# Performance work log

Measured on AMD Instinct MI355X. Metric: run time of the kernel, lower is better.

The kernel has to match this reference:

```python
import jax, jax.numpy as jnp
import numpy as np

H, W = 56, 56
N = H * W
C = 2
THETA_ALPHA = 160.0
THETA_BETA = 3.0
THETA_GAMMA = 3.0
NUM_ITERATIONS = 10


def setup_inputs() -> dict:
    key = jax.random.key(0)
    k1, k2, k3, k4 = jax.random.split(key, 4)
    inputs = jax.random.uniform(k1, (2, H, W), dtype=jnp.float32)
    # Keras 'uniform' initializer: U(-0.05, 0.05)
    sp_w = jax.random.uniform(k2, (C, C), minval=-0.05, maxval=0.05, dtype=jnp.float32)
    bl_w = jax.random.uniform(k3, (C, C), minval=-0.05, maxval=0.05, dtype=jnp.float32)
    compat = jax.random.uniform(k4, (C, C), minval=-0.05, maxval=0.05, dtype=jnp.float32)
    return {"inputs": inputs, "spatial_ker_weights": sp_w,
            "bilateral_ker_weights": bl_w, "compatibility_matrix": compat}


def _sqdist(f):
    # f: [N, D] -> [N, N] squared pairwise distances
    s = jnp.sum(f * f, axis=1)
    return s[:, None] + s[None, :] - 2.0 * (f @ f.T)


def _kernels(rgb_flat):
    # rgb_flat: [N, 3] pixel colors (0..255)
    ys, xs = jnp.meshgrid(jnp.arange(H, dtype=jnp.float32),
                          jnp.arange(W, dtype=jnp.float32), indexing="ij")
    pos = jnp.stack([xs.reshape(-1), ys.reshape(-1)], axis=1)  # [N, 2]
    # spatial (Gaussian) kernel: exp(-||p-q||^2 / (2*gamma^2))
    k_sp = jnp.exp(-0.5 * _sqdist(pos / THETA_GAMMA))
    # bilateral kernel: positions scaled by alpha, colors by beta
    f_bl = jnp.concatenate([pos / THETA_ALPHA, rgb_flat / THETA_BETA], axis=1)
    k_bl = jnp.exp(-0.5 * _sqdist(f_bl))
    return k_sp, k_bl


def reference(inputs, spatial_ker_weights, bilateral_ker_weights, compatibility_matrix):
    unary = inputs[0]            # [H, W], foreground prob
    gray = inputs[1] * 255.0     # [H, W], image intensities scaled as in the layer

    # unaries: [C, H, W] with channel 0 = 1-u, channel 1 = u
    unaries = jnp.stack([1.0 - unary, unary], axis=0).reshape(C, N)

    rgb_flat = jnp.tile(gray.reshape(-1)[:, None], (1, 3))  # [N, 3]

    k_sp, k_bl = _kernels(rgb_flat)
    ones = jnp.ones((N,), dtype=jnp.float32)
    norm_sp = k_sp @ ones  # [N]
    norm_bl = k_bl @ ones  # [N]

    q = unaries
    for i in range(NUM_ITERATIONS):
        softmax_out = q if i == 0 else jax.nn.softmax(q, axis=0)
        spatial_out = (softmax_out @ k_sp) / norm_sp[None, :]     # [C, N]
        bilateral_out = (softmax_out @ k_bl) / norm_bl[None, :]   # [C, N]
        message = spatial_ker_weights @ spatial_out + bilateral_ker_weights @ bilateral_out
        pairwise = compatibility_matrix @ message                 # [C, N]
        q = unaries - pairwise

    cur_q = q.reshape(C, H, W).transpose(1, 2, 0)  # [H, W, C]
    obj_prob = jax.nn.softmax(cur_q, axis=2)[:, :, 1]
    return obj_prob.reshape(1, H, W)
```

## Files before the change

### kernel.cpp

```cpp
#include <hip/hip_runtime.h>


namespace {

constexpr int NPIX = 3136;
constexpr int WIMG = 56;
constexpr int JPB  = 16;
constexpr int NBLK = NPIX / JPB;
constexpr int NTHR = 512;
constexpr int NQ   = NPIX / 4;
constexpr int NBUF = 9;
constexpr int BAND = 16;
constexpr int Q2   = NQ - NTHR;

constexpr float LOG2E = 1.4426950408889634f;
constexpr float C1 = -LOG2E / 18.0f;
constexpr float C2 = -LOG2E / 51200.0f;
constexpr float C3 = -LOG2E / 6.0f;

constexpr int O_SSH  = 0;
constexpr int O_GSRT = 12544;
constexpr int O_MSRT = 25088;
constexpr int O_OFF  = 31360;
constexpr int O_WSX  = 32400;
constexpr int O_WSY  = 35984;
constexpr int O_ROWC = 39568;
constexpr int POOLSZ = 43376;

#define REDUCE32(v) \
    { v += __shfl_xor(v, 1); v += __shfl_xor(v, 2); v += __shfl_xor(v, 4); \
      v += __shfl_xor(v, 8); v += __shfl_xor(v, 16); }

__global__ __launch_bounds__(NTHR) void crf_all(
    const float* __restrict__ inp,
    const float* __restrict__ spw, const float* __restrict__ blw,
    const float* __restrict__ cmw,
    float* sbufs, float* __restrict__ out)
{
    __shared__ __align__(16) unsigned char pool[POOLSZ];
    float*  s_sh  = (float*)(pool + O_SSH);
    float4* s_sh4 = (float4*)(pool + O_SSH);
    float*  g_srt = (float*)(pool + O_GSRT);
    unsigned short* m_srt = (unsigned short*)(pool + O_MSRT);
    unsigned*       offs  = (unsigned*)(pool + O_OFF);
    float*  wsx   = (float*)(pool + O_WSX);
    float*  wsy   = (float*)(pool + O_WSY);
    float*  rowc  = (float*)(pool + O_ROWC);
    unsigned short* H  = (unsigned short*)(pool + O_SSH);
    unsigned*       Hz = (unsigned*)(pool + O_SSH);

    const int t   = threadIdx.x;
    const int bid = blockIdx.x;
    const int sub = t & 31;
    const int jl  = t >> 5;
    const int j   = bid * JPB + jl;
    const int xj  = j % WIMG;
    const int yj  = j / WIMG;
    const float xjf = (float)xj, yjf = (float)yj;

    const float uj = inp[j];
    const float gj = inp[NPIX + j] * 255.0f;

    const float e0 = cmw[2] - cmw[0];
    const float e1 = cmw[3] - cmw[1];
    const float alpha = e0 * (spw[0] + blw[0]) + e1 * (spw[2] + blw[2]);
    const float beta  = e0 * (spw[1] - spw[0]) + e1 * (spw[3] - spw[2]);
    const float gamma = e0 * (blw[1] - blw[0]) + e1 * (blw[3] - blw[2]);

    for (int i = t; i < 6272; i += NTHR) Hz[i] = 0u;
    for (int idx = t; idx < JPB * 56; idx += NTHR) {
        const int jlw = idx / 56, p = idx - jlw * 56;
        const int jj = bid * JPB + jlw;
        const float ddx = (float)(jj % WIMG - p);
        const float ddy = (float)(jj / WIMG - p);
        wsx[idx] = __builtin_amdgcn_exp2f(C1 * ddx * ddx);
        wsy[idx] = __builtin_amdgcn_exp2f(C1 * ddy * ddy);
    }
    __syncthreads();
    if (t < 49) {
        unsigned short* Hr = H + t * 256;
        const int mb = t * 64;
        for (int i = 0; i < 64; ++i) {
            int b = (int)(inp[NPIX + mb + i] * 255.0f);
            b = b > 255 ? 255 : b;
            Hr[b] = (unsigned short)(Hr[b] + 1);
        }
    }
    __syncthreads();
    if (t < 256) {
        unsigned run = 0;
        for (int c = 0; c < 49; ++c) {
            unsigned short v = H[c * 256 + t];
            H[c * 256 + t] = (unsigned short)run;
            run += v;
        }
        offs[t] = run;
    }
    __syncthreads();
    if (t < 64) {
        unsigned v0 = offs[4 * t], v1 = offs[4 * t + 1];
        unsigned v2 = offs[4 * t + 2], v3 = offs[4 * t + 3];
        unsigned sum = v0 + v1 + v2 + v3;
        unsigned sc = sum;
        for (int d = 1; d < 64; d <<= 1) {
            unsigned n = __shfl_up(sc, d);
            if (t >= d) sc += n;
        }
        unsigned base = sc - sum;
        offs[4 * t] = base;
        offs[4 * t + 1] = base + v0;
        offs[4 * t + 2] = base + v0 + v1;
        offs[4 * t + 3] = base + v0 + v1 + v2;
        if (t == 63) offs[256] = sc;
    }
    __syncthreads();
    if (t < 49) {
        unsigned short* Hr = H + t * 256;
        const int mb = t * 64;
        for (int i = 0; i < 64; ++i) {
            int b = (int)(inp[NPIX + mb + i] * 255.0f);
            b = b > 255 ? 255 : b;
            int r = (int)offs[b] + (int)Hr[b];
            Hr[b] = (unsigned short)(Hr[b] + 1);
            m_srt[r] = (unsigned short)(mb + i);
        }
    }
    __syncthreads();
    for (int p = t; p < NPIX; p += NTHR)
        g_srt[p] = inp[NPIX + (int)m_srt[p]] * 255.0f;
    {
        const float4* u4 = (const float4*)inp;
        for (int q = t; q < NQ; q += NTHR) s_sh4[q] = u4[q];
    }
    __syncthreads();

    float sx, sy;
    {
        float dd = xjf - (float)sub;
        sx = __builtin_amdgcn_exp2f(C1 * dd * dd);
        if (sub + 32 < 56) {
            float d2 = xjf - (float)(sub + 32);
            sx += __builtin_amdgcn_exp2f(C1 * d2 * d2);
        }
        REDUCE32(sx);
        dd = yjf - (float)sub;
        sy = __builtin_amdgcn_exp2f(C1 * dd * dd);
        if (sub + 32 < 56) {
            float d2 = yjf - (float)(sub + 32);
            sy += __builtin_amdgcn_exp2f(C1 * d2 * d2);
        }
        REDUCE32(sy);
    }
    const float rnsp = 1.0f / (sx * sy);

    int bj = (int)gj; bj = bj > 255 ? 255 : bj;
    const int blo = (int)offs[bj < BAND ? 0 : bj - BAND];
    const int bhi = (int)offs[(bj + BAND > 255 ? 255 : bj + BAND) + 1];

    auto spatial = [&]() -> float {
        const int wv = t >> 6;
        const int ln = t & 63;
        if (ln < 56) {
            const float4* S = s_sh4 + ln * 14;
            float4 sv[14];
#pragma unroll
            for (int q = 0; q < 14; ++q) sv[q] = S[q];
#pragma unroll
            for (int cc = 0; cc < 2; ++cc) {
                const int c = wv * 2 + cc;
                const float4* R = (const float4*)(wsx + c * 56);
                float acc = 0.f;
#pragma unroll
                for (int q = 0; q < 14; ++q) {
                    float4 w = R[q];
                    acc = fmaf(w.x, sv[q].x, acc); acc = fmaf(w.y, sv[q].y, acc);
                    acc = fmaf(w.z, sv[q].z, acc); acc = fmaf(w.w, sv[q].w, acc);
                }
                rowc[ln * 17 + c] = acc;
            }
        }
        __syncthreads();
        const float* wy = wsy + jl * 56;
        float part = wy[sub] * rowc[sub * 17 + jl];
        if (sub + 32 < 56)
            part = fmaf(wy[sub + 32], rowc[(sub + 32) * 17 + jl], part);
        REDUCE32(part);
        return part;
    };

    auto bilateral = [&](float* nacc_out) -> float {
        float acc = 0.f, nacc = 0.f;
        for (int p = blo + sub; p < bhi; p += 32) {
            const int m = (int)m_srt[p];
            const float gv = g_srt[p];
            const float sv = s_sh[m];
            const int yi = (m * 9363) >> 19;
            const int xi = m - yi * 56;
            const float ux = (float)xi - xjf, vy = (float)yi - yjf;
            const float r2 = fmaf(ux, ux, vy * vy);
            const float dg = gv - gj;
            const float w = __builtin_amdgcn_exp2f(fmaf(dg * C3, dg, r2 * C2));
            acc = fmaf(w, sv, acc);
            if (nacc_out) nacc += w;
        }
        REDUCE32(acc);
        if (nacc_out) { REDUCE32(nacc); *nacc_out = nacc; }
        return acc;
    };

    auto publish_sync = [&](float s, float* buf) {
        if (sub == 0)
            __hip_atomic_store(&buf[j], s, __ATOMIC_RELAXED,
                               __HIP_MEMORY_SCOPE_AGENT);
        const float4* src = (const float4*)buf;
        float4 a, b;
        const bool two = (t < Q2);
        bool da = false, db = !two;
        for (;;) {
            if (!da)
                asm volatile("global_load_dwordx4 %0, %1, off sc0 sc1"
                             : "=&v"(a) : "v"(src + t));
            if (!db)
                asm volatile("global_load_dwordx4 %0, %1, off sc0 sc1"
                             : "=&v"(b) : "v"(src + NTHR + t));
            asm volatile("s_waitcnt vmcnt(0)" ::: "memory");
            if (!da) da = (fminf(fminf(a.x, a.y), fminf(a.z, a.w)) != 0.0f);
            if (!db) db = (fminf(fminf(b.x, b.y), fminf(b.z, b.w)) != 0.0f);
            if (da && db) break;
        }
        s_sh4[t] = a;
        if (two) s_sh4[NTHR + t] = b;
        __syncthreads();
    };

    const float base = 2.0f * uj - 1.0f - alpha;
    float rnbl, s;

    {
        float tsp = spatial();
        float nacc;
        float acc = bilateral(&nacc);
        rnbl = 1.0f / nacc;
        float d = base - beta * (tsp * rnsp) - gamma * (acc * rnbl);
        s = 1.0f / (1.0f + __builtin_amdgcn_exp2f(-d * LOG2E));
    }
    publish_sync(s, sbufs);

    for (int k = 1; k < 10; ++k) {
        float tsp = spatial();
        float acc = bilateral(nullptr);
        float d = base - beta * (tsp * rnsp) - gamma * (acc * rnbl);
        s = 1.0f / (1.0f + __builtin_amdgcn_exp2f(-d * LOG2E));
        if (k < 9) publish_sync(s, sbufs + k * NPIX);
        else if (sub == 0) out[j] = s;
    }
}

}

extern "C" void kernel_launch(void* const* d_in, const int* in_sizes, int n_in,
                              void* d_out, int out_size, void* d_ws, size_t ws_size,
                              hipStream_t stream) {
    const float* inp = (const float*)d_in[0];
    const float* spw = (const float*)d_in[1];
    const float* blw = (const float*)d_in[2];
    const float* cmw = (const float*)d_in[3];
    float* sbufs = (float*)d_ws;
    float* out = (float*)d_out;

    hipMemsetAsync(sbufs, 0, NBUF * NPIX * sizeof(float), stream);
    crf_all<<<dim3(NBLK), dim3(NTHR), 0, stream>>>(inp, spw, blw, cmw,
                                                   sbufs, out);
}
```

Before: 66.02 us.

## Coarsen intensity bins, single-pass sort, sync-free spatial reduce, unroll bilateral loop

The counting sort moves to 128 two-level bins. Each pixel's local rank is recorded during the histogram pass, so the second serial scatter pass becomes a parallel scatter over all threads. The spatial separable filter now does the y-weighting in registers and reduces with 64-wide shuffles, which removes the rowc shared buffer and a block-wide barrier per call. The bilateral band loop is unrolled by four to raise memory-level parallelism. The coarser bins widen the intensity band slightly, adding some extra bilateral work.

Result: faster. 63.72 us (-3.5%).

```diff
diff --git a/kernel.cpp b/kernel.cpp
--- a/kernel.cpp
+++ b/kernel.cpp
@@ -10,8 +10,11 @@
 constexpr int NTHR = 512;
 constexpr int NQ   = NPIX / 4;
 constexpr int NBUF = 9;
-constexpr int BAND = 16;
 constexpr int Q2   = NQ - NTHR;
+constexpr int NBIN = 128;
+constexpr int BANDB = 9;
+constexpr int NCHK = 98;
+constexpr int CPX  = 32;
 
 constexpr float LOG2E = 1.4426950408889634f;
 constexpr float C1 = -LOG2E / 18.0f;
@@ -22,14 +25,17 @@
 constexpr int O_GSRT = 12544;
 constexpr int O_MSRT = 25088;
 constexpr int O_OFF  = 31360;
-constexpr int O_WSX  = 32400;
-constexpr int O_WSY  = 35984;
-constexpr int O_ROWC = 39568;
-constexpr int POOLSZ = 43376;
+constexpr int O_WSX  = 31888;
+constexpr int O_WSY  = 35472;
+constexpr int O_LIDX = 39056;
+constexpr int POOLSZ = 42192;
 
 #define REDUCE32(v) \
     { v += __shfl_xor(v, 1); v += __shfl_xor(v, 2); v += __shfl_xor(v, 4); \
       v += __shfl_xor(v, 8); v += __shfl_xor(v, 16); }
+#define REDUCE64(v) \
+    { v += __shfl_xor(v, 1); v += __shfl_xor(v, 2); v += __shfl_xor(v, 4); \
+      v += __shfl_xor(v, 8); v += __shfl_xor(v, 16); v += __shfl_xor(v, 32); }
 
 __global__ __launch_bounds__(NTHR) void crf_all(
     const float* __restrict__ inp,
@@ -45,7 +51,7 @@
     unsigned*       offs  = (unsigned*)(pool + O_OFF);
     float*  wsx   = (float*)(pool + O_WSX);
     float*  wsy   = (float*)(pool + O_WSY);
-    float*  rowc  = (float*)(pool + O_ROWC);
+    unsigned char*  lidx = (unsigned char*)(pool + O_LIDX);
     unsigned short* H  = (unsigned short*)(pool + O_SSH);
     unsigned*       Hz = (unsigned*)(pool + O_SSH);
 
@@ -77,53 +83,46 @@
         wsy[idx] = __builtin_amdgcn_exp2f(C1 * ddy * ddy);
     }
     __syncthreads();
-    if (t < 49) {
-        unsigned short* Hr = H + t * 256;
-        const int mb = t * 64;
-        for (int i = 0; i < 64; ++i) {
+    if (t < NCHK) {
+        unsigned short* Hr = H + t * NBIN;
+        const int mb = t * CPX;
+        for (int i = 0; i < CPX; ++i) {
             int b = (int)(inp[NPIX + mb + i] * 255.0f);
-            b = b > 255 ? 255 : b;
+            b = (b > 255 ? 255 : b) >> 1;
+            lidx[mb + i] = (unsigned char)Hr[b];
             Hr[b] = (unsigned short)(Hr[b] + 1);
         }
     }
     __syncthreads();
-    if (t < 256) {
+    if (t < NBIN) {
         unsigned run = 0;
-        for (int c = 0; c < 49; ++c) {
-            unsigned short v = H[c * 256 + t];
-            H[c * 256 + t] = (unsigned short)run;
+        for (int c = 0; c < NCHK; ++c) {
+            unsigned short v = H[c * NBIN + t];
+            H[c * NBIN + t] = (unsigned short)run;
             run += v;
         }
         offs[t] = run;
     }
     __syncthreads();
     if (t < 64) {
-        unsigned v0 = offs[4 * t], v1 = offs[4 * t + 1];
-        unsigned v2 = offs[4 * t + 2], v3 = offs[4 * t + 3];
-        unsigned sum = v0 + v1 + v2 + v3;
+        unsigned v0 = offs[2 * t], v1 = offs[2 * t + 1];
+        unsigned sum = v0 + v1;
         unsigned sc = sum;
         for (int d = 1; d < 64; d <<= 1) {
             unsigned n = __shfl_up(sc, d);
             if (t >= d) sc += n;
         }
         unsigned base = sc - sum;
-        offs[4 * t] = base;
-        offs[4 * t + 1] = base + v0;
-        offs[4 * t + 2] = base + v0 + v1;
-        offs[4 * t + 3] = base + v0 + v1 + v2;
-        if (t == 63) offs[256] = sc;
-    }
-    __syncthreads();
-    if (t < 49) {
-        unsigned short* Hr = H + t * 256;
-        const int mb = t * 64;
-        for (int i = 0; i < 64; ++i) {
-            int b = (int)(inp[NPIX + mb + i] * 255.0f);
-            b = b > 255 ? 255 : b;
-            int r = (int)offs[b] + (int)Hr[b];
-            Hr[b] = (unsigned short)(Hr[b] + 1);
-            m_srt[r] = (unsigned short)(mb + i);
-        }
+        offs[2 * t] = base;
+        offs[2 * t + 1] = base + v0;
+        if (t == 63) offs[NBIN] = sc;
+    }
+    __syncthreads();
+    for (int m = t; m < NPIX; m += NTHR) {
+        int b = (int)(inp[NPIX + m] * 255.0f);
+        b = (b > 255 ? 255 : b) >> 1;
+        const int r = (int)offs[b] + (int)H[(m >> 5) * NBIN + b] + (int)lidx[m];
+        m_srt[r] = (unsigned short)m;
     }
     __syncthreads();
     for (int p = t; p < NPIX; p += NTHR)
@@ -153,56 +152,69 @@
     }
     const float rnsp = 1.0f / (sx * sy);
 
-    int bj = (int)gj; bj = bj > 255 ? 255 : bj;
-    const int blo = (int)offs[bj < BAND ? 0 : bj - BAND];
-    const int bhi = (int)offs[(bj + BAND > 255 ? 255 : bj + BAND) + 1];
+    int bj = (int)gj; bj = (bj > 255 ? 255 : bj) >> 1;
+    const int b0 = bj < BANDB ? 0 : bj - BANDB;
+    const int b1 = bj + BANDB > NBIN - 1 ? NBIN - 1 : bj + BANDB;
+    const int blo = (int)offs[b0];
+    const int bhi = (int)offs[b1 + 1];
 
     auto spatial = [&]() -> float {
         const int wv = t >> 6;
         const int ln = t & 63;
+        float v0 = 0.f, v1 = 0.f;
         if (ln < 56) {
             const float4* S = s_sh4 + ln * 14;
             float4 sv[14];
 #pragma unroll
             for (int q = 0; q < 14; ++q) sv[q] = S[q];
+            const int c0 = wv * 2, c1 = c0 + 1;
+            const float4* R0 = (const float4*)(wsx + c0 * 56);
+            const float4* R1 = (const float4*)(wsx + c1 * 56);
+            float a0 = 0.f, a1 = 0.f;
 #pragma unroll
-            for (int cc = 0; cc < 2; ++cc) {
-                const int c = wv * 2 + cc;
-                const float4* R = (const float4*)(wsx + c * 56);
-                float acc = 0.f;
-#pragma unroll
-                for (int q = 0; q < 14; ++q) {
-                    float4 w = R[q];
-                    acc = fmaf(w.x, sv[q].x, acc); acc = fmaf(w.y, sv[q].y, acc);
-                    acc = fmaf(w.z, sv[q].z, acc); acc = fmaf(w.w, sv[q].w, acc);
-                }
-                rowc[ln * 17 + c] = acc;
+            for (int q = 0; q < 14; ++q) {
+                float4 w0 = R0[q], w1 = R1[q];
+                a0 = fmaf(w0.x, sv[q].x, a0); a0 = fmaf(w0.y, sv[q].y, a0);
+                a0 = fmaf(w0.z, sv[q].z, a0); a0 = fmaf(w0.w, sv[q].w, a0);
+                a1 = fmaf(w1.x, sv[q].x, a1); a1 = fmaf(w1.y, sv[q].y, a1);
+                a1 = fmaf(w1.z, sv[q].z, a1); a1 = fmaf(w1.w, sv[q].w, a1);
             }
-        }
-        __syncthreads();
-        const float* wy = wsy + jl * 56;
-        float part = wy[sub] * rowc[sub * 17 + jl];
-        if (sub + 32 < 56)
-            part = fmaf(wy[sub + 32], rowc[(sub + 32) * 17 + jl], part);
-        REDUCE32(part);
-        return part;
+            v0 = wsy[c0 * 56 + ln] * a0;
+            v1 = wsy[c1 * 56 + ln] * a1;
+        }
+        REDUCE64(v0); REDUCE64(v1);
+        return (ln < 32) ? v0 : v1;
     };
 
     auto bilateral = [&](float* nacc_out) -> float {
         float acc = 0.f, nacc = 0.f;
-        for (int p = blo + sub; p < bhi; p += 32) {
-            const int m = (int)m_srt[p];
-            const float gv = g_srt[p];
-            const float sv = s_sh[m];
-            const int yi = (m * 9363) >> 19;
-            const int xi = m - yi * 56;
-            const float ux = (float)xi - xjf, vy = (float)yi - yjf;
-            const float r2 = fmaf(ux, ux, vy * vy);
-            const float dg = gv - gj;
-            const float w = __builtin_amdgcn_exp2f(fmaf(dg * C3, dg, r2 * C2));
-            acc = fmaf(w, sv, acc);
-            if (nacc_out) nacc += w;
-        }
+        int p = blo + sub;
+#define BIL_BODY(MM, GG, SS) { \
+            const int yi = (MM * 9363) >> 19; \
+            const int xi = MM - yi * 56; \
+            const float ux = (float)xi - xjf, vy = (float)yi - yjf; \
+            const float r2 = fmaf(ux, ux, vy * vy); \
+            const float dg = GG - gj; \
+            const float w = __builtin_amdgcn_exp2f(fmaf(dg * C3, dg, r2 * C2)); \
+            acc = fmaf(w, SS, acc); \
+            if (nacc_out) nacc += w; }
+        for (; p + 96 < bhi; p += 128) {
+            const int m0 = m_srt[p],      m1 = m_srt[p + 32];
+            const int m2 = m_srt[p + 64], m3 = m_srt[p + 96];
+            const float g0 = g_srt[p],      g1 = g_srt[p + 32];
+            const float g2 = g_srt[p + 64], g3 = g_srt[p + 96];
+            const float s0 = s_sh[m0], s1 = s_sh[m1];
+            const float s2 = s_sh[m2], s3 = s_sh[m3];
+            BIL_BODY(m0, g0, s0) BIL_BODY(m1, g1, s1)
+            BIL_BODY(m2, g2, s2) BIL_BODY(m3, g3, s3)
+        }
+        for (; p < bhi; p += 32) {
+            const int mm = (int)m_srt[p];
+            const float gg = g_srt[p];
+            const float ss = s_sh[mm];
+            BIL_BODY(mm, gg, ss)
+        }
+#undef BIL_BODY
         REDUCE32(acc);
         if (nacc_out) { REDUCE32(nacc); *nacc_out = nacc; }
         return acc;
```
